# Kernel optimization log

Measured on AMD Instinct MI355X. Metric: run time of the kernel, lower is better.

Reference implementation:

```python
import jax, jax.numpy as jnp
import numpy as np

DIM = 128
N_NODES = 100000
N_EDGES = 640000


def setup_inputs() -> dict:
    key = jax.random.key(0)
    k1, k2, k3, k4, k5, k6 = jax.random.split(key, 6)
    x = jax.random.normal(k1, (N_NODES, DIM), dtype=jnp.float32)
    edge_index = jax.random.randint(k2, (2, N_EDGES), 0, N_NODES, dtype=jnp.int64)
    edge_weight = jax.random.uniform(k3, (N_EDGES,), dtype=jnp.float32)
    # Linear(dim, dim) params (PyTorch stores weight as [out, in])
    bound = 1.0 / np.sqrt(DIM)
    W = jax.random.uniform(k4, (DIM, DIM), minval=-bound, maxval=bound, dtype=jnp.float32)
    b = jax.random.uniform(k5, (DIM,), minval=-bound, maxval=bound, dtype=jnp.float32)
    alpha = jnp.float32(0.5)
    return {"x": x, "edge_index": edge_index, "num_nodes": N_NODES,
            "edge_weight": edge_weight, "W": W, "b": b, "alpha": alpha}


def reference(x, edge_index, num_nodes, edge_weight, W, b, alpha):
    src = edge_index[0]
    dst = edge_index[1]
    msg = x[src] * edge_weight[:, None]                      # [E, D] gather + weight
    agg = jax.ops.segment_sum(msg, dst, num_segments=num_nodes)   # [N, D] scatter-add
    deg = jax.ops.segment_sum(jnp.ones_like(edge_weight), dst, num_segments=num_nodes)
    deg = jnp.maximum(deg, 1.0)                              # clamp(min=1.0)
    agg = agg / deg[:, None]                                 # mean normalization
    return x + alpha * (agg @ W.T + b)                       # linear + alpha residual
```

## Files before the change

kernel.cpp:

```cpp
#include <hip/hip_runtime.h>
#include <hip/hip_bf16.h>

#define DIM 128
#define NPB 512
#define NPB_SHIFT 9

#define FROWS 64
#define FPAD 136

typedef __attribute__((ext_vector_type(8))) short bf16x8;
typedef __attribute__((ext_vector_type(8))) unsigned short u16x8;
typedef __attribute__((ext_vector_type(4))) float f32x4;

__device__ __forceinline__ short f2bf(float f) {
    union { __hip_bfloat16 h; short s; } u;
    u.h = __float2bfloat16(f);
    return u.s;
}
__device__ __forceinline__ float bf2f(unsigned short s) {
    union { unsigned int u; float f; } c;
    c.u = ((unsigned int)s) << 16;
    return c.f;
}

__device__ __forceinline__ int load_dst(const void* eidx, int flag64, int E, int e) {
    return flag64 ? (int)((const long long*)eidx)[E + e] : ((const int*)eidx)[E + e];
}
__device__ __forceinline__ int load_src(const void* eidx, int flag64, int E, int e) {
    return flag64 ? (int)((const long long*)eidx)[e] : ((const int*)eidx)[e];
}

__global__ __launch_bounds__(256) void prep_kernel(
        const float* __restrict__ x, unsigned short* __restrict__ xb, int n8,
        int* __restrict__ gcnt, int nzero,
        const unsigned int* __restrict__ e, int* __restrict__ flags) {
    int stride = gridDim.x * blockDim.x;
    int t0 = blockIdx.x * blockDim.x + threadIdx.x;
    for (int t = t0; t < nzero; t += stride) gcnt[t] = 0;
    for (int t = t0; t < n8; t += stride) {
        const float4* pp = (const float4*)(x + (size_t)t * 8);
        float4 a = pp[0], b = pp[1];
        u16x8 o;
        o[0] = (unsigned short)f2bf(a.x); o[1] = (unsigned short)f2bf(a.y);
        o[2] = (unsigned short)f2bf(a.z); o[3] = (unsigned short)f2bf(a.w);
        o[4] = (unsigned short)f2bf(b.x); o[5] = (unsigned short)f2bf(b.y);
        o[6] = (unsigned short)f2bf(b.z); o[7] = (unsigned short)f2bf(b.w);
        *(u16x8*)(xb + (size_t)t * 8) = o;
    }
    if (blockIdx.x == 0 && threadIdx.x == 0) {
        int ok64 = 1;
        for (int t = 0; t < 128; ++t) {
            if (e[2 * t + 1] != 0u) { ok64 = 0; break; }
        }
        flags[0] = ok64;
    }
}

__global__ __launch_bounds__(256) void histb_kernel(
        const void* __restrict__ eidx, int* __restrict__ gcnt,
        const int* __restrict__ flags, int E, int NB) {
    __shared__ int bcnt[256];
    const int tid = threadIdx.x;
    bcnt[tid] = 0;
    __syncthreads();
    int f = flags[0];
    int stride = gridDim.x * blockDim.x;
    for (int e = blockIdx.x * blockDim.x + tid; e < E; e += stride)
        atomicAdd(&bcnt[load_dst(eidx, f, E, e) >> NPB_SHIFT], 1);
    __syncthreads();
    if (tid < NB && bcnt[tid] > 0) atomicAdd(&gcnt[tid], bcnt[tid]);
}

__global__ __launch_bounds__(256) void scanb_kernel(
        const int* __restrict__ gcnt, int* __restrict__ gstart,
        int* __restrict__ gcursor, int NB, int E) {
    __shared__ int s[256];
    const int tid = threadIdx.x;
    int val = (tid < NB) ? gcnt[tid] : 0;
    s[tid] = val;
    __syncthreads();
    for (int off = 1; off < 256; off <<= 1) {
        int t = (tid >= off) ? s[tid - off] : 0;
        __syncthreads();
        s[tid] += t;
        __syncthreads();
    }
    int excl = s[tid] - val;
    if (tid < NB) { gstart[tid] = excl; gcursor[tid] = excl; }
    if (tid == NB) gstart[NB] = E;
}

#define A1_EPT 16
#define A1_EPB (256 * A1_EPT)
__global__ __launch_bounds__(256) void part_kernel(
        const void* __restrict__ eidx, const float* __restrict__ ew,
        int* __restrict__ gcursor, unsigned long long* __restrict__ srcw_tmp,
        const int* __restrict__ flags, int E) {
    __shared__ unsigned long long stage[A1_EPB];
    __shared__ unsigned char sbid[A1_EPB];
    __shared__ int bcnt[256], bscan[256], bcur[256], brun[256];
    const int tid = threadIdx.x;
    const int base = blockIdx.x * A1_EPB;
    const int f = flags[0];

    bcnt[tid] = 0;
    __syncthreads();

    unsigned long long pk[A1_EPT];
    unsigned char bid[A1_EPT];
    #pragma unroll
    for (int i = 0; i < A1_EPT; ++i) {
        int e = base + tid + i * 256;
        bid[i] = 0xFF;
        if (e < E) {
            int src = load_src(eidx, f, E, e);
            int dst = load_dst(eidx, f, E, e);
            unsigned int w = __float_as_uint(ew[e]);
            int b = dst >> NPB_SHIFT;
            pk[i] = ((unsigned long long)w << 26)
                  | ((unsigned long long)(dst & (NPB - 1)) << 17)
                  | (unsigned long long)(unsigned)src;
            bid[i] = (unsigned char)b;
            atomicAdd(&bcnt[b], 1);
        }
    }
    __syncthreads();

    int val = bcnt[tid];
    bscan[tid] = val;
    __syncthreads();
    for (int off = 1; off < 256; off <<= 1) {
        int t = (tid >= off) ? bscan[tid - off] : 0;
        __syncthreads();
        bscan[tid] += t;
        __syncthreads();
    }
    int excl = bscan[tid] - val;
    __syncthreads();
    bscan[tid] = excl;
    bcur[tid] = excl;
    __syncthreads();

    #pragma unroll
    for (int i = 0; i < A1_EPT; ++i) {
        if (bid[i] != 0xFF) {
            int slot = atomicAdd(&bcur[bid[i]], 1);
            stage[slot] = pk[i];
            sbid[slot] = bid[i];
        }
    }
    if (bcnt[tid] > 0) brun[tid] = atomicAdd(&gcursor[tid], bcnt[tid]);
    __syncthreads();

    int tot = (base + A1_EPB <= E) ? A1_EPB : (E - base);
    for (int s = tid; s < tot; s += 256) {
        int b = sbid[s];
        srcw_tmp[brun[b] + (s - bscan[b])] = stage[s];
    }
}

__global__ __launch_bounds__(256) void sort_kernel(
        const unsigned long long* __restrict__ srcw_tmp,
        const int* __restrict__ gstart, unsigned long long* __restrict__ srcw,
        int* __restrict__ rowstart, int nn) {
    __shared__ int cnt[NPB], excl[NPB], cur[NPB], hs[256];
    const int tid = threadIdx.x;
    const int b = blockIdx.x;
    const int node0 = b << NPB_SHIFT;
    const int e0 = gstart[b], e1 = gstart[b + 1];

    cnt[tid] = 0; cnt[tid + 256] = 0;
    __syncthreads();
    for (int e = e0 + tid; e < e1; e += 256)
        atomicAdd(&cnt[(int)((srcw_tmp[e] >> 17) & (NPB - 1))], 1);
    __syncthreads();

    int c0 = cnt[2 * tid], c1 = cnt[2 * tid + 1];
    int ps = c0 + c1;
    hs[tid] = ps;
    __syncthreads();
    for (int off = 1; off < 256; off <<= 1) {
        int t = (tid >= off) ? hs[tid - off] : 0;
        __syncthreads();
        hs[tid] += t;
        __syncthreads();
    }
    int pexcl = hs[tid] - ps;
    excl[2 * tid] = pexcl;
    excl[2 * tid + 1] = pexcl + c0;
    cur[2 * tid] = pexcl;
    cur[2 * tid + 1] = pexcl + c0;
    __syncthreads();

    int nbn = nn - node0; if (nbn > NPB) nbn = NPB;
    for (int t = tid; t < nbn; t += 256)
        rowstart[node0 + t] = e0 + excl[t];

    for (int e = e0 + tid; e < e1; e += 256) {
        unsigned long long pk = srcw_tmp[e];
        int dl = (int)((pk >> 17) & (NPB - 1));
        int pos = e0 + atomicAdd(&cur[dl], 1);
        srcw[pos] = ((pk >> 26) << 32) | (pk & 0x1FFFFULL);
    }
}

__global__ __launch_bounds__(256) void gather_kernel(
        const unsigned short* __restrict__ xb, const uint2* __restrict__ srcw,
        const int* __restrict__ rowstart, unsigned short* __restrict__ aggb,
        int nn, int E) {
    int g = (blockIdx.x * blockDim.x + threadIdx.x) >> 4;
    int sub16 = threadIdx.x & 15;
    if (g >= nn) return;
    int n0 = rowstart[g];
    int n1 = (g + 1 < nn) ? rowstart[g + 1] : E;
    float acc[8] = {0.f, 0.f, 0.f, 0.f, 0.f, 0.f, 0.f, 0.f};
    int e = n0;
    for (; e + 4 <= n1; e += 4) {
        uint2 sw0 = srcw[e];
        uint2 sw1 = srcw[e + 1];
        uint2 sw2 = srcw[e + 2];
        uint2 sw3 = srcw[e + 3];
        u16x8 x0 = *(const u16x8*)(xb + (size_t)sw0.x * DIM + sub16 * 8);
        u16x8 x1 = *(const u16x8*)(xb + (size_t)sw1.x * DIM + sub16 * 8);
        u16x8 x2 = *(const u16x8*)(xb + (size_t)sw2.x * DIM + sub16 * 8);
        u16x8 x3 = *(const u16x8*)(xb + (size_t)sw3.x * DIM + sub16 * 8);
        float w0 = __uint_as_float(sw0.y);
        float w1 = __uint_as_float(sw1.y);
        float w2 = __uint_as_float(sw2.y);
        float w3 = __uint_as_float(sw3.y);
        #pragma unroll
        for (int j = 0; j < 8; ++j) {
            acc[j] = fmaf(bf2f(x0[j]), w0, acc[j]);
            acc[j] = fmaf(bf2f(x1[j]), w1, acc[j]);
            acc[j] = fmaf(bf2f(x2[j]), w2, acc[j]);
            acc[j] = fmaf(bf2f(x3[j]), w3, acc[j]);
        }
    }
    for (; e < n1; ++e) {
        uint2 sw = srcw[e];
        u16x8 xr = *(const u16x8*)(xb + (size_t)sw.x * DIM + sub16 * 8);
        float w = __uint_as_float(sw.y);
        #pragma unroll
        for (int j = 0; j < 8; ++j) acc[j] = fmaf(bf2f(xr[j]), w, acc[j]);
    }
    float inv = 1.0f / fmaxf((float)(n1 - n0), 1.0f);
    u16x8 o;
    #pragma unroll
    for (int j = 0; j < 8; ++j) o[j] = (unsigned short)f2bf(acc[j] * inv);
    *(u16x8*)(aggb + (size_t)g * DIM + sub16 * 8) = o;
}

__global__ __launch_bounds__(512) void finish_kernel(
        const unsigned short* __restrict__ aggb, float* __restrict__ out,
        const float* __restrict__ x, const float* __restrict__ W,
        const float* __restrict__ bias, const float* __restrict__ alphaP, int nn) {
    __shared__ alignas(16) unsigned short A_lds[FROWS * FPAD];
    const int tid  = threadIdx.x;
    const int wv   = tid >> 6;
    const int lane = tid & 63;
    const int half = lane >> 4;
    const int l16  = lane & 15;
    const int b0   = blockIdx.x * FROWS;
    const float alpha = alphaP[0];

    const int jcol = wv * 16 + l16;
    bf16x8 bfrag[4];
    #pragma unroll
    for (int kt = 0; kt < 4; ++kt) {
        const float4* w4 = (const float4*)(W + (size_t)jcol * DIM + kt * 32 + half * 8);
        float4 lo = w4[0], hi = w4[1];
        bf16x8 b;
        b[0] = f2bf(lo.x); b[1] = f2bf(lo.y); b[2] = f2bf(lo.z); b[3] = f2bf(lo.w);
        b[4] = f2bf(hi.x); b[5] = f2bf(hi.y); b[6] = f2bf(hi.z); b[7] = f2bf(hi.w);
        bfrag[kt] = b;
    }
    const float bias_j = bias[jcol];

    #pragma unroll
    for (int it = 0; it < 2; ++it) {
        int p = it * 512 + tid;
        int row = p >> 4;
        int c8 = p & 15;
        int node = b0 + row;
        u16x8 v = {0, 0, 0, 0, 0, 0, 0, 0};
        if (node < nn) v = *(const u16x8*)(aggb + (size_t)node * DIM + c8 * 8);
        *(u16x8*)&A_lds[row * FPAD + c8 * 8] = v;
    }
    __syncthreads();

    #pragma unroll
    for (int mt = 0; mt < 4; ++mt) {
        f32x4 acc = {0.f, 0.f, 0.f, 0.f};
        #pragma unroll
        for (int kt = 0; kt < 4; ++kt) {
            const bf16x8 a = *(const bf16x8*)&A_lds[(mt * 16 + l16) * FPAD + kt * 32 + half * 8];
            acc = __builtin_amdgcn_mfma_f32_16x16x32_bf16(a, bfrag[kt], acc, 0, 0, 0);
        }
        #pragma unroll
        for (int r = 0; r < 4; ++r) {
            int grow = b0 + mt * 16 + half * 4 + r;
            if (grow < nn) {
                size_t idx = (size_t)grow * DIM + jcol;
                out[idx] = x[idx] + alpha * (acc[r] + bias_j);
            }
        }
    }
}

extern "C" void kernel_launch(void* const* d_in, const int* in_sizes, int n_in,
                              void* d_out, int out_size, void* d_ws, size_t ws_size,
                              hipStream_t stream) {
    const float* x      = (const float*)d_in[0];
    const void*  eidx   = d_in[1];
    const float* ew     = (const float*)d_in[3];
    const float* W      = (const float*)d_in[4];
    const float* bias   = (const float*)d_in[5];
    const float* alphaP = (const float*)d_in[6];

    const int NN = in_sizes[0] / DIM;
    const int E  = in_sizes[3];
    const int NB = (NN + NPB - 1) / NPB;

    unsigned short* aggb = (unsigned short*)d_ws;
    unsigned long long* srcw     = (unsigned long long*)(aggb + (size_t)NN * DIM);
    unsigned long long* srcw_tmp = srcw + E;
    int* rowstart = (int*)(srcw_tmp + E);
    int* gcnt     = rowstart + NN;
    int* gstart   = gcnt + 256;
    int* gcursor  = gstart + 257;
    int* flags    = gcursor + 256;

    unsigned short* xb = (unsigned short*)d_out;
    float* out = (float*)d_out;

    int n8 = NN * DIM / 8;
    prep_kernel<<<2048, 256, 0, stream>>>(x, xb, n8, gcnt, 256,
                                          (const unsigned int*)eidx, flags);

    histb_kernel<<<1024, 256, 0, stream>>>(eidx, gcnt, flags, E, NB);

    scanb_kernel<<<1, 256, 0, stream>>>(gcnt, gstart, gcursor, NB, E);

    int a1blocks = (E + A1_EPB - 1) / A1_EPB;
    part_kernel<<<a1blocks, 256, 0, stream>>>(eidx, ew, gcursor, srcw_tmp, flags, E);

    sort_kernel<<<NB, 256, 0, stream>>>(srcw_tmp, gstart, srcw, rowstart, NN);

    int gblocks = (NN + 15) / 16;
    gather_kernel<<<gblocks, 256, 0, stream>>>(xb, (const uint2*)srcw, rowstart,
                                               aggb, NN, E);

    int fblocks = (NN + FROWS - 1) / FROWS;
    finish_kernel<<<fblocks, 512, 0, stream>>>(aggb, out, x, W, bias, alphaP, NN);
}
```

Measured before the change: 126.6 us.

## Fuse histogram into conversion pass, widen sort block, read bf16 residual

Merges the destination-bucket histogram into the fp32-to-bf16 conversion kernel and moves counter zeroing and index-width detection into a small init kernel. Halves edges per block in partitioning, runs the per-bucket sort with 512 threads and a single-element scan, and stores the bf16 copy of x in workspace instead of the output buffer. The final residual add now reads bf16 x rather than fp32 x, cutting residual read bandwidth at the cost of rounding the residual term, which may exceed accuracy tolerance.

```diff
diff --git a/kernel.cpp b/kernel.cpp
--- a/kernel.cpp
+++ b/kernel.cpp
@@ -30,13 +30,35 @@
     return flag64 ? (int)((const long long*)eidx)[e] : ((const int*)eidx)[e];
 }
 
+__global__ __launch_bounds__(256) void init_kernel(
+        int* __restrict__ gcnt, const unsigned int* __restrict__ e,
+        int* __restrict__ flags) {
+    gcnt[threadIdx.x] = 0;
+    if (threadIdx.x == 0) {
+        int ok64 = 1;
+        for (int t = 0; t < 128; ++t) {
+            if (e[2 * t + 1] != 0u) { ok64 = 0; break; }
+        }
+        flags[0] = ok64;
+    }
+}
+
 __global__ __launch_bounds__(256) void prep_kernel(
         const float* __restrict__ x, unsigned short* __restrict__ xb, int n8,
-        int* __restrict__ gcnt, int nzero,
-        const unsigned int* __restrict__ e, int* __restrict__ flags) {
-    int stride = gridDim.x * blockDim.x;
-    int t0 = blockIdx.x * blockDim.x + threadIdx.x;
-    for (int t = t0; t < nzero; t += stride) gcnt[t] = 0;
+        const void* __restrict__ eidx, int* __restrict__ gcnt,
+        const int* __restrict__ flags, int E, int NB) {
+    __shared__ int bcnt[256];
+    const int tid = threadIdx.x;
+    bcnt[tid] = 0;
+    __syncthreads();
+
+    const int stride = gridDim.x * blockDim.x;
+    const int t0 = blockIdx.x * blockDim.x + tid;
+    const int f = flags[0];
+
+    for (int e = t0; e < E; e += stride)
+        atomicAdd(&bcnt[load_dst(eidx, f, E, e) >> NPB_SHIFT], 1);
+
     for (int t = t0; t < n8; t += stride) {
         const float4* pp = (const float4*)(x + (size_t)t * 8);
         float4 a = pp[0], b = pp[1];
@@ -47,26 +69,7 @@
         o[6] = (unsigned short)f2bf(b.z); o[7] = (unsigned short)f2bf(b.w);
         *(u16x8*)(xb + (size_t)t * 8) = o;
     }
-    if (blockIdx.x == 0 && threadIdx.x == 0) {
-        int ok64 = 1;
-        for (int t = 0; t < 128; ++t) {
-            if (e[2 * t + 1] != 0u) { ok64 = 0; break; }
-        }
-        flags[0] = ok64;
-    }
-}
-
-__global__ __launch_bounds__(256) void histb_kernel(
-        const void* __restrict__ eidx, int* __restrict__ gcnt,
-        const int* __restrict__ flags, int E, int NB) {
-    __shared__ int bcnt[256];
-    const int tid = threadIdx.x;
-    bcnt[tid] = 0;
-    __syncthreads();
-    int f = flags[0];
-    int stride = gridDim.x * blockDim.x;
-    for (int e = blockIdx.x * blockDim.x + tid; e < E; e += stride)
-        atomicAdd(&bcnt[load_dst(eidx, f, E, e) >> NPB_SHIFT], 1);
+
     __syncthreads();
     if (tid < NB && bcnt[tid] > 0) atomicAdd(&gcnt[tid], bcnt[tid]);
 }
@@ -90,7 +93,7 @@
     if (tid == NB) gstart[NB] = E;
 }
 
-#define A1_EPT 16
+#define A1_EPT 8
 #define A1_EPB (256 * A1_EPT)
 __global__ __launch_bounds__(256) void part_kernel(
         const void* __restrict__ eidx, const float* __restrict__ ew,
@@ -159,44 +162,39 @@
     }
 }
 
-__global__ __launch_bounds__(256) void sort_kernel(
+__global__ __launch_bounds__(512) void sort_kernel(
         const unsigned long long* __restrict__ srcw_tmp,
         const int* __restrict__ gstart, unsigned long long* __restrict__ srcw,
         int* __restrict__ rowstart, int nn) {
-    __shared__ int cnt[NPB], excl[NPB], cur[NPB], hs[256];
+    __shared__ int cnt[NPB], cur[NPB], s[NPB];
     const int tid = threadIdx.x;
     const int b = blockIdx.x;
     const int node0 = b << NPB_SHIFT;
     const int e0 = gstart[b], e1 = gstart[b + 1];
 
-    cnt[tid] = 0; cnt[tid + 256] = 0;
-    __syncthreads();
-    for (int e = e0 + tid; e < e1; e += 256)
+    cnt[tid] = 0;
+    __syncthreads();
+    for (int e = e0 + tid; e < e1; e += 512)
         atomicAdd(&cnt[(int)((srcw_tmp[e] >> 17) & (NPB - 1))], 1);
     __syncthreads();
 
-    int c0 = cnt[2 * tid], c1 = cnt[2 * tid + 1];
-    int ps = c0 + c1;
-    hs[tid] = ps;
-    __syncthreads();
-    for (int off = 1; off < 256; off <<= 1) {
-        int t = (tid >= off) ? hs[tid - off] : 0;
-        __syncthreads();
-        hs[tid] += t;
-        __syncthreads();
-    }
-    int pexcl = hs[tid] - ps;
-    excl[2 * tid] = pexcl;
-    excl[2 * tid + 1] = pexcl + c0;
-    cur[2 * tid] = pexcl;
-    cur[2 * tid + 1] = pexcl + c0;
+    int val = cnt[tid];
+    s[tid] = val;
+    __syncthreads();
+    for (int off = 1; off < 512; off <<= 1) {
+        int t = (tid >= off) ? s[tid - off] : 0;
+        __syncthreads();
+        s[tid] += t;
+        __syncthreads();
+    }
+    int excl = s[tid] - val;
+    cur[tid] = excl;
     __syncthreads();
 
     int nbn = nn - node0; if (nbn > NPB) nbn = NPB;
-    for (int t = tid; t < nbn; t += 256)
-        rowstart[node0 + t] = e0 + excl[t];
-
-    for (int e = e0 + tid; e < e1; e += 256) {
+    if (tid < nbn) rowstart[node0 + tid] = e0 + excl;
+
+    for (int e = e0 + tid; e < e1; e += 512) {
         unsigned long long pk = srcw_tmp[e];
         int dl = (int)((pk >> 17) & (NPB - 1));
         int pos = e0 + atomicAdd(&cur[dl], 1);
@@ -252,7 +250,7 @@
 
 __global__ __launch_bounds__(512) void finish_kernel(
         const unsigned short* __restrict__ aggb, float* __restrict__ out,
-        const float* __restrict__ x, const float* __restrict__ W,
+        const unsigned short* __restrict__ xb, const float* __restrict__ W,
         const float* __restrict__ bias, const float* __restrict__ alphaP, int nn) {
     __shared__ alignas(16) unsigned short A_lds[FROWS * FPAD];
     const int tid  = threadIdx.x;
@@ -301,7 +299,7 @@
             int grow = b0 + mt * 16 + half * 4 + r;
             if (grow < nn) {
                 size_t idx = (size_t)grow * DIM + jcol;
-                out[idx] = x[idx] + alpha * (acc[r] + bias_j);
+                out[idx] = bf2f(xb[idx]) + alpha * (acc[r] + bias_j);
             }
         }
     }
@@ -322,7 +320,8 @@
     const int NB = (NN + NPB - 1) / NPB;
 
     unsigned short* aggb = (unsigned short*)d_ws;
-    unsigned long long* srcw     = (unsigned long long*)(aggb + (size_t)NN * DIM);
+    unsigned short* xb   = aggb + (size_t)NN * DIM;
+    unsigned long long* srcw     = (unsigned long long*)(xb + (size_t)NN * DIM);
     unsigned long long* srcw_tmp = srcw + E;
     int* rowstart = (int*)(srcw_tmp + E);
     int* gcnt     = rowstart + NN;
@@ -330,26 +329,24 @@
     int* gcursor  = gstart + 257;
     int* flags    = gcursor + 256;
 
-    unsigned short* xb = (unsigned short*)d_out;
     float* out = (float*)d_out;
 
+    init_kernel<<<1, 256, 0, stream>>>(gcnt, (const unsigned int*)eidx, flags);
+
     int n8 = NN * DIM / 8;
-    prep_kernel<<<2048, 256, 0, stream>>>(x, xb, n8, gcnt, 256,
-                                          (const unsigned int*)eidx, flags);
-
-    histb_kernel<<<1024, 256, 0, stream>>>(eidx, gcnt, flags, E, NB);
+    prep_kernel<<<2048, 256, 0, stream>>>(x, xb, n8, eidx, gcnt, flags, E, NB);
 
     scanb_kernel<<<1, 256, 0, stream>>>(gcnt, gstart, gcursor, NB, E);
 
     int a1blocks = (E + A1_EPB - 1) / A1_EPB;
     part_kernel<<<a1blocks, 256, 0, stream>>>(eidx, ew, gcursor, srcw_tmp, flags, E);
 
-    sort_kernel<<<NB, 256, 0, stream>>>(srcw_tmp, gstart, srcw, rowstart, NN);
+    sort_kernel<<<NB, 512, 0, stream>>>(srcw_tmp, gstart, srcw, rowstart, NN);
 
     int gblocks = (NN + 15) / 16;
     gather_kernel<<<gblocks, 256, 0, stream>>>(xb, (const uint2*)srcw, rowstart,
                                                aggb, NN, E);
 
     int fblocks = (NN + FROWS - 1) / FROWS;
-    finish_kernel<<<fblocks, 512, 0, stream>>>(aggb, out, x, W, bias, alphaP, NN);
-}
+    finish_kernel<<<fblocks, 512, 0, stream>>>(aggb, out, xb, W, bias, alphaP, NN);
+}
```

Measured after the change: 139.8 us. +10.5%, slower.
